# Optimization experiments

Hardware: AMD Instinct MI355X
Metric: run time of the kernel (lower is better)

The kernel has to match this reference:

```python
import jax, jax.numpy as jnp
import numpy as np

DIM = 1024
B, S = 2, 2048

def _gelu(v):
    return jax.nn.gelu(v, approximate=False)

def setup_inputs() -> dict:
    key = jax.random.key(0)
    ks = jax.random.split(key, 24)
    d = DIM
    def lin(k, fan_in, fan_out):
        k1, k2 = jax.random.split(k)
        bound = 1.0 / np.sqrt(fan_in)
        W = jax.random.uniform(k1, (fan_in, fan_out), jnp.float32, -bound, bound)
        b = jax.random.uniform(k2, (fan_out,), jnp.float32, -bound, bound)
        return W, b
    w_pt1, b_pt1 = lin(ks[0], d, 2 * d)
    w_pt2, b_pt2 = lin(ks[1], 2 * d, d)
    w_wg, b_wg = lin(ks[2], d, d)
    w_mag, b_mag = lin(ks[3], d, d)
    w_q1, b_q1 = lin(ks[4], d, d)
    w_q2, b_q2 = lin(ks[5], d, d)
    w_mix, b_mix = lin(ks[6], d, 2 * d)
    w_o1, b_o1 = lin(ks[7], d, d)
    w_o2, b_o2 = lin(ks[8], d, d)
    return {
        "x": jax.random.normal(ks[9], (B, S, d), jnp.float32),
        "w_pt1": w_pt1, "b_pt1": b_pt1, "w_pt2": w_pt2, "b_pt2": b_pt2,
        "int_scale": jnp.ones((d,), jnp.float32) * 0.001,
        "w_wg": w_wg, "b_wg": b_wg,
        "gate_temp": jnp.ones((1,), jnp.float32) * 2.0,
        "w_mag": w_mag, "b_mag": b_mag,
        "w_q1": w_q1, "b_q1": b_q1, "w_q2": w_q2, "b_q2": b_q2,
        "w_mix": w_mix, "b_mix": b_mix,
        "ln_g": jnp.ones((d,), jnp.float32), "ln_b": jnp.zeros((d,), jnp.float32),
        "w_o1": w_o1, "b_o1": b_o1, "w_o2": w_o2, "b_o2": b_o2,
    }

def reference(x, w_pt1, b_pt1, w_pt2, b_pt2, int_scale, w_wg, b_wg, gate_temp,
              w_mag, b_mag, w_q1, b_q1, w_q2, b_q2, w_mix, b_mix,
              ln_g, ln_b, w_o1, b_o1, w_o2, b_o2):
    # input-dependent phase basis
    phase_delta = _gelu(x @ w_pt1 + b_pt1) @ w_pt2 + b_pt2          # [B,S,D]
    phi = jnp.cumsum(phase_delta * jnp.abs(int_scale), axis=1)
    # selective write gate + magnitude
    write_gate = jax.nn.sigmoid((x @ w_wg + b_wg) * gate_temp)
    magnitude = jax.nn.sigmoid(x @ w_mag + b_mag) * 5.0
    content = write_gate * x * magnitude
    # complex-phase memory accumulation (4 seq-length scans)
    memory_real = jnp.cumsum(content * jnp.cos(phi), axis=1)
    memory_imag = jnp.cumsum(content * jnp.sin(phi), axis=1)
    accum_weight = jnp.cumsum(write_gate * magnitude + 1e-8, axis=1)
    inv_s = 1.0 / jnp.sqrt(accum_weight)
    mr, mi = memory_real * inv_s, memory_imag * inv_s
    # query-phase retrieval (complex rotation)
    query_phase = phi + (_gelu(x @ w_q1 + b_q1) @ w_q2 + b_q2)
    cq, sq = jnp.cos(query_phase), jnp.sin(query_phase)
    retrieved_real = mr * cq + mi * sq
    retrieved_imag = mi * cq - mr * sq
    # input-dependent output mixing
    mix = x @ w_mix + b_mix
    d = x.shape[-1]
    mix_real = jax.nn.sigmoid(mix[..., :d])
    mix_imag = jax.nn.sigmoid(mix[..., d:])
    retrieved = mix_real * retrieved_real + mix_imag * retrieved_imag
    # output head: LayerNorm -> Linear -> GELU -> (Dropout=identity in eval) -> Linear
    mu = jnp.mean(retrieved, axis=-1, keepdims=True)
    var = jnp.var(retrieved, axis=-1, keepdims=True)
    ln = (retrieved - mu) / jnp.sqrt(var + 1e-5) * ln_g + ln_b
    out = _gelu(ln @ w_o1 + b_o1) @ w_o2 + b_o2
    return x + out
```

## Files before the change

kernel.cpp:

```cpp
#include <hip/hip_runtime.h>
#include <hip/hip_bf16.h>

#define MTOT 4096
#define DD   1024
#define D2   2048
#define SS   2048
#define BB   2
#define NC2  64
#define CL2  (SS/NC2)

typedef __attribute__((ext_vector_type(8))) short bf16x8;
typedef __attribute__((ext_vector_type(4))) float f32x4;

__device__ __forceinline__ float sigmf(float v){
    return 1.0f/(1.0f+__expf(-v));
}
__device__ __forceinline__ float geluf(float v){
    float u = 0.7978845608f*v*(1.0f + 0.044715f*v*v);
    float e = __expf(2.0f*u);
    float t = 1.0f - 2.0f/(e + 1.0f);
    return 0.5f*v*(1.0f + t);
}
__device__ __forceinline__ ushort f2bf(float f){
    unsigned u = __float_as_uint(f);
    unsigned r = (u + 0x7FFF + ((u>>16)&1)) >> 16;
    return (ushort)r;
}
__device__ __forceinline__ float bf2f(ushort u){
    return __uint_as_float(((unsigned)u)<<16);
}

__device__ __forceinline__ void stage_tile(
    const ushort* __restrict__ A, const ushort* __restrict__ Bt, int K,
    int m0, int n0, int k0, ushort* As, ushort* Bs)
{
    int tid = threadIdx.x;
    #pragma unroll
    for (int i = 0; i < 2; i++) {
        int e = (i*256 + tid) * 8;
        int r = e >> 5;
        int s = (e >> 3) & 3;
        int c = ((s ^ ((r >> 1) & 3)) << 3);
        __builtin_amdgcn_global_load_lds(
            (const __attribute__((address_space(1))) void*)(A + (size_t)(m0 + r)*K + k0 + c),
            (__attribute__((address_space(3))) void*)(As + e), 16, 0, 0);
        __builtin_amdgcn_global_load_lds(
            (const __attribute__((address_space(1))) void*)(Bt + (size_t)(n0 + r)*K + k0 + c),
            (__attribute__((address_space(3))) void*)(Bs + e), 16, 0, 0);
    }
}

__device__ __forceinline__ void load_frags(
    const ushort* As, const ushort* Bs, int wr, int wc, int lrow, int cs,
    bf16x8 (&af)[4], bf16x8 (&bfr)[4])
{
    #pragma unroll
    for (int i = 0; i < 4; i++) {
        int ra = wr*64 + i*16 + lrow;
        int rb = wc*64 + i*16 + lrow;
        af[i]  = *(const bf16x8*)(As + ra*32 + ((cs ^ ((ra>>1)&3))<<3));
        bfr[i] = *(const bf16x8*)(Bs + rb*32 + ((cs ^ ((rb>>1)&3))<<3));
    }
}

__device__ __forceinline__ void do_mfma(
    const bf16x8 (&af)[4], const bf16x8 (&bfr)[4], f32x4 (&acc)[4][4])
{
    __builtin_amdgcn_s_setprio(1);
    #pragma unroll
    for (int i = 0; i < 4; i++)
        #pragma unroll
        for (int j = 0; j < 4; j++)
            acc[i][j] = __builtin_amdgcn_mfma_f32_16x16x32_bf16(af[i], bfr[j], acc[i][j], 0, 0, 0);
    __builtin_amdgcn_s_setprio(0);
}

__device__ __forceinline__ void mgemm_core(
    const ushort* __restrict__ A, const ushort* __restrict__ Bt, int K,
    int m0, int n0, ushort (&As)[2][4096], ushort (&Bs)[2][4096], f32x4 (&acc)[4][4])
{
    int lane = threadIdx.x & 63, wave = threadIdx.x >> 6;
    int wr = wave >> 1, wc = wave & 1;
    int lrow = lane & 15, cs = lane >> 4;
    int NT = K >> 5;
    stage_tile(A, Bt, K, m0, n0, 0,  As[0], Bs[0]);
    stage_tile(A, Bt, K, m0, n0, 32, As[1], Bs[1]);
    for (int t = 0; t < NT-1; ++t) {
        asm volatile("s_waitcnt vmcnt(4)" ::: "memory");
        __builtin_amdgcn_s_barrier();
        bf16x8 af[4], bfr[4];
        load_frags(As[t&1], Bs[t&1], wr, wc, lrow, cs, af, bfr);
        if (t < NT-2) {
            asm volatile("s_waitcnt lgkmcnt(0)" ::: "memory");
            __builtin_amdgcn_s_barrier();
            stage_tile(A, Bt, K, m0, n0, (t+2) << 5, As[t&1], Bs[t&1]);
        }
        __builtin_amdgcn_sched_barrier(0);
        do_mfma(af, bfr, acc);
    }
    asm volatile("s_waitcnt vmcnt(0)" ::: "memory");
    __builtin_amdgcn_s_barrier();
    bf16x8 af[4], bfr[4];
    load_frags(As[(NT-1)&1], Bs[(NT-1)&1], wr, wc, lrow, cs, af, bfr);
    do_mfma(af, bfr, acc);
}

__global__ __launch_bounds__(256,4) void mgemmA_k(
    const ushort* __restrict__ xb, const ushort* __restrict__ Wt,
    const float* __restrict__ b_pt1, const float* __restrict__ b_wg,
    const float* __restrict__ b_mag, const float* __restrict__ b_q1,
    const float* __restrict__ b_mix, const float* __restrict__ gtemp,
    ushort* __restrict__ H1b, ushort* __restrict__ wgb, ushort* __restrict__ magb,
    ushort* __restrict__ Hqb, ushort* __restrict__ mixb)
{
    __shared__ ushort As[2][4096], Bs[2][4096];
    int bid = blockIdx.x;
    int xcd = bid & 7, local = bid >> 3;
    int m0 = (xcd*4 + (local & 3)) * 128;
    int n0 = (local >> 2) * 128;
    f32x4 acc[4][4] = {};
    mgemm_core(xb, Wt, 1024, m0, n0, As, Bs, acc);
    int lane = threadIdx.x & 63, wave = threadIdx.x >> 6;
    int wr = wave >> 1, wc = wave & 1;
    int rng = n0 >> 10;
    float gt = gtemp[0];
    #pragma unroll
    for (int i = 0; i < 4; i++) {
        int mb = m0 + wr*64 + i*16 + (lane>>4)*4;
        #pragma unroll
        for (int j = 0; j < 4; j++) {
            int n = n0 + wc*64 + j*16 + (lane&15);
            #pragma unroll
            for (int r = 0; r < 4; r++) {
                int m = mb + r;
                float v = acc[i][j][r];
                if (rng < 2) {
                    H1b[(size_t)m*D2 + n] = f2bf(geluf(v + b_pt1[n]));
                } else if (rng == 2) {
                    wgb[(size_t)m*DD + n-2048] = f2bf(sigmf((v + b_wg[n-2048])*gt));
                } else if (rng == 3) {
                    magb[(size_t)m*DD + n-3072] = f2bf(sigmf(v + b_mag[n-3072])*5.0f);
                } else if (rng == 4) {
                    Hqb[(size_t)m*DD + n-4096] = f2bf(geluf(v + b_q1[n-4096]));
                } else {
                    mixb[(size_t)m*D2 + n-5120] = f2bf(sigmf(v + b_mix[n-5120]));
                }
            }
        }
    }
}

__global__ __launch_bounds__(256,4) void mgemmBC_k(
    const ushort* __restrict__ H1b, const ushort* __restrict__ wt_pt2,
    const ushort* __restrict__ Hqb, const ushort* __restrict__ wt_q2,
    const float* __restrict__ b_pt2, const float* __restrict__ b_q2,
    const float* __restrict__ iscale,
    float* __restrict__ pd, float* __restrict__ qadj)
{
    __shared__ ushort As[2][4096], Bs[2][4096];
    int bid = blockIdx.x;
    int xcd = bid & 7, local = bid >> 3;
    int m0 = (xcd*4 + (local & 3)) * 128;
    int rest = local >> 2;
    int z = rest >> 3;
    int n0 = (rest & 7) * 128;
    const ushort* A  = z ? Hqb   : H1b;
    const ushort* Bt = z ? wt_q2 : wt_pt2;
    const float* bias = z ? b_q2 : b_pt2;
    int K = z ? 1024 : 2048;
    float* outp = z ? qadj : pd;
    f32x4 acc[4][4] = {};
    mgemm_core(A, Bt, K, m0, n0, As, Bs, acc);
    int lane = threadIdx.x & 63, wave = threadIdx.x >> 6;
    int wr = wave >> 1, wc = wave & 1;
    #pragma unroll
    for (int i = 0; i < 4; i++) {
        int mb = m0 + wr*64 + i*16 + (lane>>4)*4;
        #pragma unroll
        for (int j = 0; j < 4; j++) {
            int n = n0 + wc*64 + j*16 + (lane&15);
            float bv = bias[n];
            float sc = z ? 1.0f : fabsf(iscale[n]);
            #pragma unroll
            for (int r = 0; r < 4; r++) {
                float v = acc[i][j][r] + bv;
                outp[(size_t)(mb+r)*DD + n] = z ? v : v*sc;
            }
        }
    }
}

template<int ACT, bool RESID, bool OUTBF16>
__global__ __launch_bounds__(256,4) void mgemm_k(
    const ushort* __restrict__ A, const ushort* __restrict__ Bt,
    const float* __restrict__ bias, const float* __restrict__ resid,
    void* __restrict__ Cout, int N, int K)
{
    __shared__ ushort As[2][4096], Bs[2][4096];
    int bid = blockIdx.x;
    int xcd = bid & 7, local = bid >> 3;
    int m0 = (xcd*4 + (local & 3)) * 128;
    int n0 = (local >> 2) * 128;
    f32x4 acc[4][4] = {};
    mgemm_core(A, Bt, K, m0, n0, As, Bs, acc);
    int lane = threadIdx.x & 63, wave = threadIdx.x >> 6;
    int wr = wave >> 1, wc = wave & 1;
    #pragma unroll
    for (int i = 0; i < 4; i++) {
        int mb = m0 + wr*64 + i*16 + (lane>>4)*4;
        #pragma unroll
        for (int j = 0; j < 4; j++) {
            int n = n0 + wc*64 + j*16 + (lane&15);
            float bv = bias[n];
            #pragma unroll
            for (int r = 0; r < 4; r++) {
                size_t idx = (size_t)(mb + r)*N + n;
                float v = acc[i][j][r] + bv;
                if (ACT==1) v = geluf(v);
                if (RESID) v += resid[idx];
                if (OUTBF16) ((ushort*)Cout)[idx] = f2bf(v);
                else         ((float*)Cout)[idx]  = v;
            }
        }
    }
}

__global__ __launch_bounds__(256) void cvt_bf16_k(const float* __restrict__ in, ushort* __restrict__ outp){
    size_t i = ((size_t)blockIdx.x*256 + threadIdx.x)*8;
    float4 a = *(const float4*)(in + i);
    float4 b = *(const float4*)(in + i + 4);
    ushort t[8];
    t[0]=f2bf(a.x); t[1]=f2bf(a.y); t[2]=f2bf(a.z); t[3]=f2bf(a.w);
    t[4]=f2bf(b.x); t[5]=f2bf(b.y); t[6]=f2bf(b.z); t[7]=f2bf(b.w);
    *(int4*)(outp + i) = *(const int4*)t;
}

__device__ __forceinline__ void tcvt_body(const float* W, ushort* Wt, int K, int N){
    __shared__ float tile[32][33];
    int n0 = blockIdx.x*32, k0 = blockIdx.y*32;
    int tx = threadIdx.x & 7, ty = threadIdx.x >> 3;
    float4 v = *(const float4*)(W + (size_t)(k0+ty)*N + n0 + tx*4);
    tile[ty][tx*4+0]=v.x; tile[ty][tx*4+1]=v.y; tile[ty][tx*4+2]=v.z; tile[ty][tx*4+3]=v.w;
    __syncthreads();
    ushort t[4];
    #pragma unroll
    for (int i=0;i<4;i++) t[i] = f2bf(tile[tx*4+i][ty]);
    *(uint2*)(Wt + (size_t)(n0+ty)*K + k0 + tx*4) = *(const uint2*)t;
}

__global__ __launch_bounds__(256) void tcvt_k(const float* __restrict__ W, ushort* __restrict__ Wt, int K, int N){
    tcvt_body(W, Wt, K, N);
}
__global__ __launch_bounds__(256) void tcvt2_k(const float* __restrict__ w0, ushort* __restrict__ o0,
                                               const float* __restrict__ w1, ushort* __restrict__ o1){
    tcvt_body(blockIdx.z ? w1 : w0, blockIdx.z ? o1 : o0, 1024, 2048);
}
__global__ __launch_bounds__(256) void tcvt6_k(
    const float* __restrict__ w0, ushort* __restrict__ o0,
    const float* __restrict__ w1, ushort* __restrict__ o1,
    const float* __restrict__ w2, ushort* __restrict__ o2,
    const float* __restrict__ w3, ushort* __restrict__ o3,
    const float* __restrict__ w4, ushort* __restrict__ o4,
    const float* __restrict__ w5, ushort* __restrict__ o5)
{
    const float* W; ushort* Wt;
    switch(blockIdx.z){
        case 0: W=w0; Wt=o0; break;
        case 1: W=w1; Wt=o1; break;
        case 2: W=w2; Wt=o2; break;
        case 3: W=w3; Wt=o3; break;
        case 4: W=w4; Wt=o4; break;
        default: W=w5; Wt=o5; break;
    }
    tcvt_body(W, Wt, 1024, 1024);
}

__global__ __launch_bounds__(256) void passA_k(
    const float* __restrict__ pd, float* __restrict__ csum)
{
    int d = blockIdx.x*256 + threadIdx.x;
    int c = blockIdx.y, b = blockIdx.z;
    const float* p = pd + ((size_t)b*SS + (size_t)c*CL2)*DD + d;
    float s = 0.f;
    for (int i = 0; i < CL2; i++) s += p[(size_t)i*DD];
    csum[((size_t)b*NC2 + c)*DD + d] = s;
}

__global__ void scan2_k(float* __restrict__ csum, int nchains){
    int idx = blockIdx.x*256 + threadIdx.x;
    if (idx >= nchains) return;
    int xg = idx / DD, d = idx % DD;
    float* p = csum + (size_t)xg*NC2*DD + d;
    float run = 0.f;
    for (int c = 0; c < NC2; c++){ float t = p[(size_t)c*DD]; p[(size_t)c*DD] = run; run += t; }
}

__global__ __launch_bounds__(256) void passB_k(
    const float* __restrict__ pd, const ushort* __restrict__ wgb,
    const ushort* __restrict__ magb, const ushort* __restrict__ xb,
    const float* __restrict__ csum_phi, float* __restrict__ csum_tri)
{
    int d = blockIdx.x*256 + threadIdx.x;
    int c = blockIdx.y, b = blockIdx.z;
    size_t off = ((size_t)b*SS + (size_t)c*CL2)*DD + d;
    float ph = csum_phi[((size_t)b*NC2 + c)*DD + d];
    float s0=0.f, s1=0.f, s2=0.f;
    for (int i = 0; i < CL2; i++){
        size_t o = off + (size_t)i*DD;
        ph += pd[o];
        float w = bf2f(wgb[o]), m = bf2f(magb[o]);
        float ct = w*bf2f(xb[o])*m;
        float sp, cp; sincosf(ph, &sp, &cp);
        s0 += ct*cp; s1 += ct*sp; s2 += fmaf(w, m, 1e-8f);
    }
    size_t cs = ((size_t)b*NC2 + c)*DD + d;
    size_t G = (size_t)BB*NC2*DD;
    csum_tri[cs]=s0; csum_tri[G+cs]=s1; csum_tri[2*G+cs]=s2;
}

__global__ __launch_bounds__(256) void passC_k(
    const float* __restrict__ pd, const ushort* __restrict__ wgb,
    const ushort* __restrict__ magb, const ushort* __restrict__ xb,
    const float* __restrict__ qadj, const ushort* __restrict__ mixb,
    const float* __restrict__ csum_phi, const float* __restrict__ csum_tri,
    ushort* __restrict__ ret)
{
    int d = blockIdx.x*256 + threadIdx.x;
    int c = blockIdx.y, b = blockIdx.z;
    size_t off = ((size_t)b*SS + (size_t)c*CL2)*DD + d;
    size_t cs = ((size_t)b*NC2 + c)*DD + d;
    size_t G = (size_t)BB*NC2*DD;
    float ph = csum_phi[cs];
    float r0 = csum_tri[cs], r1 = csum_tri[G+cs], r2 = csum_tri[2*G+cs];
    size_t row0 = (size_t)b*SS + (size_t)c*CL2;
    for (int i = 0; i < CL2; i++){
        size_t o = off + (size_t)i*DD;
        ph += pd[o];
        float w = bf2f(wgb[o]), m = bf2f(magb[o]);
        float ct = w*bf2f(xb[o])*m;
        float sp, cp; sincosf(ph, &sp, &cp);
        r0 += ct*cp; r1 += ct*sp; r2 += fmaf(w, m, 1e-8f);
        float inv = rsqrtf(r2);
        float mr = r0*inv, mi = r1*inv;
        float q = ph + qadj[o];
        float sq, cq; sincosf(q, &sq, &cq);
        float rr = mr*cq + mi*sq;
        float ri = mi*cq - mr*sq;
        size_t mb2 = (row0 + i)*D2 + d;
        ret[o] = f2bf(bf2f(mixb[mb2])*rr + bf2f(mixb[mb2+DD])*ri);
    }
}

__global__ __launch_bounds__(256) void ln_k(
    const ushort* __restrict__ ret, const float* __restrict__ ln_g,
    const float* __restrict__ ln_b, ushort* __restrict__ outp)
{
    int row = blockIdx.x;
    size_t base = (size_t)row*DD;
    float vals[4];
    float sum=0.f, sumsq=0.f;
    #pragma unroll
    for (int k = 0; k < 4; k++){
        int d = threadIdx.x + k*256;
        float v = bf2f(ret[base+d]);
        vals[k]=v; sum+=v; sumsq = fmaf(v,v,sumsq);
    }
    #pragma unroll
    for (int off=32; off; off>>=1){
        sum   += __shfl_down(sum,off);
        sumsq += __shfl_down(sumsq,off);
    }
    __shared__ float red[8];
    int lane = threadIdx.x & 63, wid = threadIdx.x >> 6;
    if (lane==0){ red[wid]=sum; red[4+wid]=sumsq; }
    __syncthreads();
    sum   = red[0]+red[1]+red[2]+red[3];
    sumsq = red[4]+red[5]+red[6]+red[7];
    float mu  = sum * (1.0f/DD);
    float var = sumsq*(1.0f/DD) - mu*mu;
    float rstd = rsqrtf(var + 1e-5f);
    #pragma unroll
    for (int k = 0; k < 4; k++){
        int d = threadIdx.x + k*256;
        outp[base+d] = f2bf((vals[k]-mu)*rstd*ln_g[d] + ln_b[d]);
    }
}

extern "C" void kernel_launch(void* const* d_in, const int* in_sizes, int n_in,
                              void* d_out, int out_size, void* d_ws, size_t ws_size,
                              hipStream_t stream)
{
    const float* x     = (const float*)d_in[0];
    const float* w_pt1 = (const float*)d_in[1];
    const float* b_pt1 = (const float*)d_in[2];
    const float* w_pt2 = (const float*)d_in[3];
    const float* b_pt2 = (const float*)d_in[4];
    const float* iscale= (const float*)d_in[5];
    const float* w_wg  = (const float*)d_in[6];
    const float* b_wg  = (const float*)d_in[7];
    const float* gtemp = (const float*)d_in[8];
    const float* w_mag = (const float*)d_in[9];
    const float* b_mag = (const float*)d_in[10];
    const float* w_q1  = (const float*)d_in[11];
    const float* b_q1  = (const float*)d_in[12];
    const float* w_q2  = (const float*)d_in[13];
    const float* b_q2  = (const float*)d_in[14];
    const float* w_mix = (const float*)d_in[15];
    const float* b_mix = (const float*)d_in[16];
    const float* ln_g  = (const float*)d_in[17];
    const float* ln_b  = (const float*)d_in[18];
    const float* w_o1  = (const float*)d_in[19];
    const float* b_o1  = (const float*)d_in[20];
    const float* w_o2  = (const float*)d_in[21];
    const float* b_o2  = (const float*)d_in[22];
    float* out = (float*)d_out;

    const size_t SZ = (size_t)MTOT*DD;
    ushort* u = (ushort*)d_ws;
    ushort* xb    = u;                 u += SZ;
    ushort* H1b   = u;                 u += 2*SZ;
    ushort* ret   = H1b;
    ushort* Hqb   = u;                 u += SZ;
    ushort* lnb   = Hqb;
    ushort* wgb   = u;                 u += SZ;
    ushort* magb  = u;                 u += SZ;
    ushort* mixb  = u;                 u += 2*SZ;
    ushort* Hob   = u;                 u += SZ;
    float*  pd    = (float*)u;         u += 2*SZ;
    float*  qadj  = (float*)u;         u += 2*SZ;
    ushort* Wt_all= u;                 u += (size_t)7168*1024;
    ushort* wt_pt2= u;                 u += (size_t)1024*2048;
    ushort* wt_q2 = u;                 u += (size_t)1024*1024;
    ushort* wt_o1 = u;                 u += (size_t)1024*1024;
    ushort* wt_o2 = u;                 u += (size_t)1024*1024;
    float* csum_phi = (float*)u;
    float* csum_tri = csum_phi + (size_t)BB*NC2*DD;

    dim3 blk(256);
    cvt_bf16_k<<<dim3(SZ/2048), blk, 0, stream>>>(x, xb);
    tcvt2_k<<<dim3(64, 32, 2), blk, 0, stream>>>(w_pt1, Wt_all, w_mix, Wt_all + (size_t)5120*1024);
    tcvt6_k<<<dim3(32, 32, 6), blk, 0, stream>>>(
        w_wg,  Wt_all + (size_t)2048*1024,
        w_mag, Wt_all + (size_t)3072*1024,
        w_q1,  Wt_all + (size_t)4096*1024,
        w_q2,  wt_q2,  w_o1, wt_o1,  w_o2, wt_o2);
    tcvt_k<<<dim3(32, 64), blk, 0, stream>>>(w_pt2, wt_pt2, 2048, 1024);
    mgemmA_k<<<dim3(1792), blk, 0, stream>>>(xb, Wt_all, b_pt1, b_wg, b_mag, b_q1, b_mix,
                                             gtemp, H1b, wgb, magb, Hqb, mixb);
    mgemmBC_k<<<dim3(512), blk, 0, stream>>>(H1b, wt_pt2, Hqb, wt_q2, b_pt2, b_q2,
                                             iscale, pd, qadj);
    passA_k<<<dim3(DD/256, NC2, BB), blk, 0, stream>>>(pd, csum_phi);
    scan2_k<<<dim3((BB*DD+255)/256), blk, 0, stream>>>(csum_phi, BB*DD);
    passB_k<<<dim3(DD/256, NC2, BB), blk, 0, stream>>>(pd, wgb, magb, xb, csum_phi, csum_tri);
    scan2_k<<<dim3((3*BB*DD+255)/256), blk, 0, stream>>>(csum_tri, 3*BB*DD);
    passC_k<<<dim3(DD/256, NC2, BB), blk, 0, stream>>>(pd, wgb, magb, xb, qadj, mixb,
                                                       csum_phi, csum_tri, ret);
    ln_k<<<dim3(MTOT), blk, 0, stream>>>(ret, ln_g, ln_b, lnb);
    mgemm_k<1,false,true><<<dim3(256), blk, 0, stream>>>(lnb, wt_o1, b_o1, nullptr, Hob, DD, DD);
    mgemm_k<0,true,false><<<dim3(256), blk, 0, stream>>>(Hob, wt_o2, b_o2, x, out, DD, DD);
}
```

Baseline: 267.2 us.

## Use 256x256 tiles with 4-stage LDS pipeline for fused input GEMM

Replaces the 128x128-tile, 256-thread, double-buffered input projection GEMM with a 256x256-tile, 512-thread kernel whose 8 waves each compute a 128x64 sub-tile. K-slices are staged through a 4-deep LDS ring using direct global-to-LDS loads and graded vmcnt waits. The goal is more reuse per loaded byte and deeper latency hiding. In exchange the kernel needs 128KB of LDS and more accumulator registers per wave, and the grid drops to 448 blocks, which lowers occupancy and can cause tail imbalance across CUs.

```diff
diff --git a/kernel.cpp b/kernel.cpp
--- a/kernel.cpp
+++ b/kernel.cpp
@@ -105,7 +105,55 @@
     do_mfma(af, bfr, acc);
 }
 
-__global__ __launch_bounds__(256,4) void mgemmA_k(
+__device__ __forceinline__ void stage256(
+    const ushort* __restrict__ A, const ushort* __restrict__ Bt, int K,
+    int m0, int n0, int k0, ushort* As, ushort* Bs)
+{
+    int tid = threadIdx.x;
+    #pragma unroll
+    for (int i = 0; i < 2; i++) {
+        int e = (i*512 + tid) * 8;
+        int r = e >> 5;
+        int s = (e >> 3) & 3;
+        int c = ((s ^ ((r >> 1) & 3)) << 3);
+        __builtin_amdgcn_global_load_lds(
+            (const __attribute__((address_space(1))) void*)(A + (size_t)(m0 + r)*K + k0 + c),
+            (__attribute__((address_space(3))) void*)(As + e), 16, 0, 0);
+        __builtin_amdgcn_global_load_lds(
+            (const __attribute__((address_space(1))) void*)(Bt + (size_t)(n0 + r)*K + k0 + c),
+            (__attribute__((address_space(3))) void*)(Bs + e), 16, 0, 0);
+    }
+}
+
+__device__ __forceinline__ void frag_read256(
+    const ushort* As, const ushort* Bs, int wr, int wc, int lrow, int cs,
+    bf16x8 (&af)[8], bf16x8 (&bfr)[4])
+{
+    #pragma unroll
+    for (int i = 0; i < 8; i++) {
+        int ra = wr*128 + i*16 + lrow;
+        af[i] = *(const bf16x8*)(As + ra*32 + ((cs ^ ((ra>>1)&3))<<3));
+    }
+    #pragma unroll
+    for (int j = 0; j < 4; j++) {
+        int rb = wc*64 + j*16 + lrow;
+        bfr[j] = *(const bf16x8*)(Bs + rb*32 + ((cs ^ ((rb>>1)&3))<<3));
+    }
+}
+
+__device__ __forceinline__ void mfma256(
+    const bf16x8 (&af)[8], const bf16x8 (&bfr)[4], f32x4 (&acc)[8][4])
+{
+    __builtin_amdgcn_s_setprio(1);
+    #pragma unroll
+    for (int i = 0; i < 8; i++)
+        #pragma unroll
+        for (int j = 0; j < 4; j++)
+            acc[i][j] = __builtin_amdgcn_mfma_f32_16x16x32_bf16(af[i], bfr[j], acc[i][j], 0, 0, 0);
+    __builtin_amdgcn_s_setprio(0);
+}
+
+__global__ __launch_bounds__(512,2) void mgemmA256_k(
     const ushort* __restrict__ xb, const ushort* __restrict__ Wt,
     const float* __restrict__ b_pt1, const float* __restrict__ b_wg,
     const float* __restrict__ b_mag, const float* __restrict__ b_q1,
@@ -113,20 +161,51 @@
     ushort* __restrict__ H1b, ushort* __restrict__ wgb, ushort* __restrict__ magb,
     ushort* __restrict__ Hqb, ushort* __restrict__ mixb)
 {
-    __shared__ ushort As[2][4096], Bs[2][4096];
+    __shared__ ushort As[4][8192], Bs[4][8192];
+    const int K = 1024, NT = 32;
     int bid = blockIdx.x;
     int xcd = bid & 7, local = bid >> 3;
-    int m0 = (xcd*4 + (local & 3)) * 128;
-    int n0 = (local >> 2) * 128;
-    f32x4 acc[4][4] = {};
-    mgemm_core(xb, Wt, 1024, m0, n0, As, Bs, acc);
+    int m0 = (xcd*2 + (local & 1)) * 256;
+    int n0 = (local >> 1) * 256;
     int lane = threadIdx.x & 63, wave = threadIdx.x >> 6;
-    int wr = wave >> 1, wc = wave & 1;
+    int wr = wave >> 2, wc = wave & 3;
+    int lrow = lane & 15, cs = lane >> 4;
+    f32x4 acc[8][4] = {};
+    stage256(xb, Wt, K, m0, n0, 0,  As[0], Bs[0]);
+    stage256(xb, Wt, K, m0, n0, 32, As[1], Bs[1]);
+    stage256(xb, Wt, K, m0, n0, 64, As[2], Bs[2]);
+    stage256(xb, Wt, K, m0, n0, 96, As[3], Bs[3]);
+    bf16x8 af[8]; bf16x8 bfr[4];
+    for (int t = 0; t < NT-3; ++t) {
+        asm volatile("s_waitcnt vmcnt(12)" ::: "memory");
+        __builtin_amdgcn_s_barrier();
+        frag_read256(As[t&3], Bs[t&3], wr, wc, lrow, cs, af, bfr);
+        if (t < NT-4) {
+            asm volatile("s_waitcnt lgkmcnt(0)" ::: "memory");
+            __builtin_amdgcn_s_barrier();
+            stage256(xb, Wt, K, m0, n0, (t+4) << 5, As[t&3], Bs[t&3]);
+        }
+        __builtin_amdgcn_sched_barrier(0);
+        mfma256(af, bfr, acc);
+    }
+    asm volatile("s_waitcnt vmcnt(8)" ::: "memory");
+    __builtin_amdgcn_s_barrier();
+    frag_read256(As[(NT-3)&3], Bs[(NT-3)&3], wr, wc, lrow, cs, af, bfr);
+    mfma256(af, bfr, acc);
+    asm volatile("s_waitcnt vmcnt(4)" ::: "memory");
+    __builtin_amdgcn_s_barrier();
+    frag_read256(As[(NT-2)&3], Bs[(NT-2)&3], wr, wc, lrow, cs, af, bfr);
+    mfma256(af, bfr, acc);
+    asm volatile("s_waitcnt vmcnt(0)" ::: "memory");
+    __builtin_amdgcn_s_barrier();
+    frag_read256(As[(NT-1)&3], Bs[(NT-1)&3], wr, wc, lrow, cs, af, bfr);
+    mfma256(af, bfr, acc);
+
     int rng = n0 >> 10;
     float gt = gtemp[0];
     #pragma unroll
-    for (int i = 0; i < 4; i++) {
-        int mb = m0 + wr*64 + i*16 + (lane>>4)*4;
+    for (int i = 0; i < 8; i++) {
+        int mb = m0 + wr*128 + i*16 + (lane>>4)*4;
         #pragma unroll
         for (int j = 0; j < 4; j++) {
             int n = n0 + wc*64 + j*16 + (lane&15);
@@ -445,8 +524,8 @@
         w_q1,  Wt_all + (size_t)4096*1024,
         w_q2,  wt_q2,  w_o1, wt_o1,  w_o2, wt_o2);
     tcvt_k<<<dim3(32, 64), blk, 0, stream>>>(w_pt2, wt_pt2, 2048, 1024);
-    mgemmA_k<<<dim3(1792), blk, 0, stream>>>(xb, Wt_all, b_pt1, b_wg, b_mag, b_q1, b_mix,
-                                             gtemp, H1b, wgb, magb, Hqb, mixb);
+    mgemmA256_k<<<dim3(448), dim3(512), 0, stream>>>(xb, Wt_all, b_pt1, b_wg, b_mag, b_q1, b_mix,
+                                                     gtemp, H1b, wgb, magb, Hqb, mixb);
     mgemmBC_k<<<dim3(512), blk, 0, stream>>>(H1b, wt_pt2, Hqb, wt_q2, b_pt2, b_q2,
                                              iscale, pd, qadj);
     passA_k<<<dim3(DD/256, NC2, BB), blk, 0, stream>>>(pd, csum_phi);
```

Result: slower. 381.0 us (+42.6%).
